# Optimization experiments

Hardware: AMD Instinct MI355X
Metric: run time of the kernel (lower is better)

The kernel has to match this reference:

```python
import jax, jax.numpy as jnp
import numpy as np

VOCAB, EMBED, HIDDEN = 32000, 256, 64
B, T = 4096, 64


def setup_inputs() -> dict:
    key = jax.random.key(0)
    ks = jax.random.split(key, 6)
    s = 1.0 / float(np.sqrt(HIDDEN))  # PyTorch LSTM init scale
    x = jax.random.randint(ks[0], (B, T), 0, VOCAB)
    embed_table = jax.random.normal(ks[1], (VOCAB, EMBED), jnp.float32)
    W_ih = jax.random.uniform(ks[2], (4 * HIDDEN, EMBED), jnp.float32, -s, s)
    W_hh = jax.random.uniform(ks[3], (4 * HIDDEN, HIDDEN), jnp.float32, -s, s)
    b_ih = jax.random.uniform(ks[4], (4 * HIDDEN,), jnp.float32, -s, s)
    b_hh = jax.random.uniform(ks[5], (4 * HIDDEN,), jnp.float32, -s, s)
    return {"x": x, "embed_table": embed_table, "W_ih": W_ih, "W_hh": W_hh, "b_ih": b_ih, "b_hh": b_hh}


def reference(x, embed_table, W_ih, W_hh, b_ih, b_hh):
    # Embedding lookup: [B,T,E]
    emb = embed_table[x]
    # Precompute input projection for all timesteps (PyTorch gate order i,f,g,o)
    xg = jnp.einsum('bte,ge->btg', emb, W_ih) + (b_ih + b_hh)  # [B,T,4H]
    xg = jnp.swapaxes(xg, 0, 1)  # [T,B,4H]
    h0 = jnp.zeros((x.shape[0], HIDDEN), xg.dtype)
    c0 = jnp.zeros((x.shape[0], HIDDEN), xg.dtype)

    def step(carry, xt):
        h, c = carry
        g = xt + h @ W_hh.T  # [B,4H]
        i, f, gg, o = jnp.split(g, 4, axis=-1)
        c = jax.nn.sigmoid(f) * c + jax.nn.sigmoid(i) * jnp.tanh(gg)
        h = jax.nn.sigmoid(o) * jnp.tanh(c)
        return (h, c), None

    (h, _), _ = jax.lax.scan(step, (h0, c0), xg)
    return h  # [B, HIDDEN] == hidden.squeeze(0)
```

## Files before the change

### kernel.cpp

```cpp
#include <hip/hip_runtime.h>
#include <math.h>

#define B_ 4096
#define T_ 64
#define E_ 256
#define H_ 64
#define V_ 32000
#define THREADS 512

typedef __attribute__((ext_vector_type(8))) short bf16x8;
typedef __attribute__((ext_vector_type(4))) float f32x4;
typedef __attribute__((ext_vector_type(4))) unsigned int u32x4;

__device__ __forceinline__ short f2bf(float x) {
    unsigned u = __float_as_uint(x);
    return (short)((u + 0x7FFFu + ((u >> 16) & 1u)) >> 16);
}
__device__ __forceinline__ unsigned cvt_pk_bf16(float lo, float hi) {
    unsigned r;
    asm("v_cvt_pk_bf16_f32 %0, %1, %2" : "=v"(r) : "v"(lo), "v"(hi));
    return r;
}
__device__ __forceinline__ float exp2_raw(float x) {
    float r; asm("v_exp_f32 %0, %1" : "=v"(r) : "v"(x)); return r;
}
__device__ __forceinline__ float rcp_raw(float x) {
    float r; asm("v_rcp_f32 %0, %1" : "=v"(r) : "v"(x)); return r;
}
#define LOG2E 1.442695041f

template <int CTRL>
__device__ __forceinline__ float dpp_f(float x) {
    return __int_as_float(
        __builtin_amdgcn_mov_dpp(__float_as_int(x), CTRL, 0xF, 0xF, true));
}

__device__ __forceinline__ void gld16(const void* g, void* l) {
    __builtin_amdgcn_global_load_lds(
        (const __attribute__((address_space(1))) void*)g,
        (__attribute__((address_space(3))) void*)l, 16, 0, 0);
}

__global__ void prep_kernel(const float* __restrict__ W_ih,
                            const float* __restrict__ W_hh,
                            const float* __restrict__ b_ih,
                            const float* __restrict__ b_hh,
                            const float* __restrict__ emb_table,
                            short* __restrict__ wih_frag,
                            short* __restrict__ whh_g,
                            float* __restrict__ bias_f,
                            short* __restrict__ emb_bf,
                            int tabN) {
    int tid = blockIdx.x * blockDim.x + threadIdx.x;
    int stride = gridDim.x * blockDim.x;
    for (int i = tid; i < 65536; i += stride) {
        int jj = i & 7;
        int l  = (i >> 3) & 63;
        int kc = (i >> 9) & 7;
        int tl = (i >> 12) & 1;
        int vv = i >> 13;
        int uu = (l & 15) >> 1, pp = l & 1;
        int g = tl * 128 + pp * 64 + vv * 8 + uu;
        int k = kc * 32 + (l >> 4) * 8 + jj;
        wih_frag[i] = f2bf(W_ih[g * E_ + k]);
    }
    for (int i = tid; i < 256 * 64; i += stride) whh_g[i] = f2bf(W_hh[i]);
    for (int i = tid; i < 256; i += stride) bias_f[i] = b_ih[i] + b_hh[i];
    for (int i = tid; i < (tabN >> 2); i += stride) {
        float4 v = ((const float4*)emb_table)[i];
        uint2 w;
        w.x = cvt_pk_bf16(v.x, v.y);
        w.y = cvt_pk_bf16(v.z, v.w);
        ((uint2*)emb_bf)[i] = w;
    }
}

template <int TAB>
__global__ __attribute__((amdgpu_flat_work_group_size(THREADS, THREADS),
                          amdgpu_waves_per_eu(2, 2)))
void lstm_f(const int* __restrict__ x,
            const float* __restrict__ embf,
            const short* __restrict__ embb,
            const short* __restrict__ wih_frag,
            const short* __restrict__ whh_g,
            const float* __restrict__ bias_f,
            float* __restrict__ out) {
    __shared__ __align__(16) short s_ef[4][4096];
    __shared__ __align__(16) short s_hf[2][1024];
    __shared__ int s_idx[1024];

    const int tid  = threadIdx.x;
    const int lane = tid & 63;
    const int wave = tid >> 6;
    const int r0   = blockIdx.x * 16;

    {
        const int tt = tid & 63;
        const int mA = tid >> 6;
        s_idx[tt * 16 + mA]     = x[(r0 + mA) * T_ + tt];
        s_idx[tt * 16 + mA + 8] = x[(r0 + mA + 8) * T_ + tt];
    }
    ((int*)s_hf)[tid]       = 0;
    ((int*)s_hf)[tid + 512] = 0;

    const int p  = lane & 1;
    const int c4 = lane >> 4;
    const int u  = (lane & 15) >> 1;
    const float scl2 = p ? 1.0f : 2.0f;
    const float offB = p ? 0.0f : -1.0f;
    const float enB  = -LOG2E * scl2;
    const int m0 = c4 * 4 + p * 2;

    bf16x8 wA[8], wB[8], qA0, qA1, qB0, qB1;
    float bA, bB;
    int hw_s;
    {
        const short* wp = wih_frag + wave * 8192 + lane * 8;
        #pragma unroll
        for (int kc = 0; kc < 8; ++kc) {
            wA[kc] = *(const bf16x8*)(wp + kc * 512);
            wB[kc] = *(const bf16x8*)(wp + 4096 + kc * 512);
        }
        const int gA = p * 64 + wave * 8 + u;
        const short* qp = whh_g + gA * 64 + c4 * 8;
        qA0 = *(const bf16x8*)(qp);
        qA1 = *(const bf16x8*)(qp + 32);
        qB0 = *(const bf16x8*)(qp + 8192);
        qB1 = *(const bf16x8*)(qp + 8192 + 32);
        bA = bias_f[gA];
        bB = bias_f[gA + 128];
        hw_s = (wave >> 2) * 512 + (wave & 3) * 128
             + ((u & 1) ? (m0 + 1) * 8 + (u - 1) : m0 * 8 + u);
    }

    const int m16   = lane & 15;
    const int sbase = wave * 512 + lane * 8;
    const int skoff = wave * 32 + (lane >> 4) * 8;

    __syncthreads();

    #pragma unroll
    for (int tt = 0; tt < 3; ++tt) {
        int tok = s_idx[tt * 16 + m16];
        if (TAB) {
            gld16(embb + (size_t)tok * E_ + skoff, &s_ef[tt][wave * 512]);
        } else {
            const float* pr = embf + (size_t)tok * E_ + skoff;
            float4 f0 = *(const float4*)pr;
            float4 f1 = *(const float4*)(pr + 4);
            u32x4 w;
            w[0] = cvt_pk_bf16(f0.x, f0.y);
            w[1] = cvt_pk_bf16(f0.z, f0.w);
            w[2] = cvt_pk_bf16(f1.x, f1.y);
            w[3] = cvt_pk_bf16(f1.z, f1.w);
            *(u32x4*)(&s_ef[tt][0] + sbase) = w;
        }
    }
    if (TAB) {
        asm volatile("s_waitcnt vmcnt(1) lgkmcnt(0)" ::: "memory");
        __builtin_amdgcn_s_barrier();
        __builtin_amdgcn_sched_barrier(0);
    } else {
        __syncthreads();
    }

    float c0 = 0.f, c1 = 0.f, h0v = 0.f, h1v = 0.f;
    f32x4 a0, a1, b0, b1;

    {
        a0 = (f32x4){bA, bA, bA, bA};
        b0 = (f32x4){bB, bB, bB, bB};
        a1 = (f32x4){0.f, 0.f, 0.f, 0.f};
        b1 = (f32x4){0.f, 0.f, 0.f, 0.f};
        const short* eb = &s_ef[0][0] + lane * 8;
        #pragma unroll
        for (int kc = 0; kc < 4; ++kc) {
            bf16x8 av = *(const bf16x8*)(eb + kc * 512);
            bf16x8 aw = *(const bf16x8*)(eb + (kc + 4) * 512);
            a0 = __builtin_amdgcn_mfma_f32_16x16x32_bf16(av, wA[kc], a0, 0, 0, 0);
            b0 = __builtin_amdgcn_mfma_f32_16x16x32_bf16(av, wB[kc], b0, 0, 0, 0);
            a1 = __builtin_amdgcn_mfma_f32_16x16x32_bf16(aw, wA[kc + 4], a1, 0, 0, 0);
            b1 = __builtin_amdgcn_mfma_f32_16x16x32_bf16(aw, wB[kc + 4], b1, 0, 0, 0);
        }
    }

    auto gates_phase = [&](const float* ga, const float* gb, int t) {
        float sA[4], Bv[4];
        #pragma unroll
        for (int q = 0; q < 4; ++q) {
            sA[q] = rcp_raw(1.0f + exp2_raw(-LOG2E * ga[q]));
            Bv[q] = rcp_raw(1.0f + exp2_raw(enB * gb[q])) * scl2 + offB;
        }
        float s1 = p ? sA[0] : sA[2] * Bv[2];
        float r1 = dpp_f<0xB1>(s1);
        float s2 = p ? sA[1] : sA[3] * Bv[3];
        float r2 = dpp_f<0xB1>(s2);
        float r3 = dpp_f<0xB1>(Bv[0]);
        float r4 = dpp_f<0xB1>(Bv[1]);
        float fc0 = p ? sA[2] : r1;
        float ic0 = p ? r1 : sA[0] * Bv[0];
        float oc0 = p ? Bv[2] : r3;
        float fc1 = p ? sA[3] : r2;
        float ic1 = p ? r2 : sA[1] * Bv[1];
        float oc1 = p ? Bv[3] : r4;
        c0 = fc0 * c0 + ic0;
        c1 = fc1 * c1 + ic1;
        h0v = oc0 * (1.0f - 2.0f * rcp_raw(1.0f + exp2_raw(2.0f * LOG2E * c0)));
        h1v = oc1 * (1.0f - 2.0f * rcp_raw(1.0f + exp2_raw(2.0f * LOG2E * c1)));
        float snd = (u & 1) ? h0v : h1v;
        float rcv = dpp_f<0x4E>(snd);
        unsigned hw = (u & 1) ? cvt_pk_bf16(rcv, h1v) : cvt_pk_bf16(h0v, rcv);
        *(unsigned*)(&s_hf[(t + 1) & 1][0] + hw_s) = hw;
    };

    auto p_phase = [&](int t) {
        a0 = (f32x4){bA, bA, bA, bA};
        b0 = (f32x4){bB, bB, bB, bB};
        a1 = (f32x4){0.f, 0.f, 0.f, 0.f};
        b1 = (f32x4){0.f, 0.f, 0.f, 0.f};
        const short* eb = &s_ef[(t + 1) & 3][0] + lane * 8;
        __builtin_amdgcn_s_setprio(1);
        #pragma unroll
        for (int kc = 0; kc < 4; ++kc) {
            bf16x8 av = *(const bf16x8*)(eb + kc * 512);
            bf16x8 aw = *(const bf16x8*)(eb + (kc + 4) * 512);
            a0 = __builtin_amdgcn_mfma_f32_16x16x32_bf16(av, wA[kc], a0, 0, 0, 0);
            b0 = __builtin_amdgcn_mfma_f32_16x16x32_bf16(av, wB[kc], b0, 0, 0, 0);
            a1 = __builtin_amdgcn_mfma_f32_16x16x32_bf16(aw, wA[kc + 4], a1, 0, 0, 0);
            b1 = __builtin_amdgcn_mfma_f32_16x16x32_bf16(aw, wB[kc + 4], b1, 0, 0, 0);
        }
        __builtin_amdgcn_s_setprio(0);
    };

    #pragma unroll 4
    for (int t = 0; t < T_; ++t) {
        {
            const int ts = (t + 3 < T_) ? t + 3 : T_ - 1;
            int tok = s_idx[ts * 16 + m16];
            if (TAB) {
                gld16(embb + (size_t)tok * E_ + skoff,
                      &s_ef[(t + 3) & 3][wave * 512]);
            } else {
                const float* pr = embf + (size_t)tok * E_ + skoff;
                float4 f0 = *(const float4*)pr;
                float4 f1 = *(const float4*)(pr + 4);
                u32x4 w;
                w[0] = cvt_pk_bf16(f0.x, f0.y);
                w[1] = cvt_pk_bf16(f0.z, f0.w);
                w[2] = cvt_pk_bf16(f1.x, f1.y);
                w[3] = cvt_pk_bf16(f1.z, f1.w);
                *(u32x4*)(&s_ef[(t + 3) & 3][0] + sbase) = w;
            }
        }

        const short* hb = &s_hf[t & 1][0] + lane * 8;
        bf16x8 hv0 = *(const bf16x8*)(hb);
        bf16x8 hv1 = *(const bf16x8*)(hb + 512);
        __builtin_amdgcn_s_setprio(1);
        a0 = __builtin_amdgcn_mfma_f32_16x16x32_bf16(hv0, qA0, a0, 0, 0, 0);
        a1 = __builtin_amdgcn_mfma_f32_16x16x32_bf16(hv1, qA1, a1, 0, 0, 0);
        b0 = __builtin_amdgcn_mfma_f32_16x16x32_bf16(hv0, qB0, b0, 0, 0, 0);
        b1 = __builtin_amdgcn_mfma_f32_16x16x32_bf16(hv1, qB1, b1, 0, 0, 0);
        __builtin_amdgcn_s_setprio(0);

        float ga[4], gb[4];
        #pragma unroll
        for (int q = 0; q < 4; ++q) {
            ga[q] = a0[q] + a1[q];
            gb[q] = b0[q] + b1[q];
        }

        if (wave < 4) {
            gates_phase(ga, gb, t);
            if (t < T_ - 1) p_phase(t);
        } else {
            __builtin_amdgcn_sched_barrier(0);
            if (t < T_ - 1) p_phase(t);
            __builtin_amdgcn_sched_barrier(0);
            gates_phase(ga, gb, t);
        }

        if (TAB) {
            asm volatile("s_waitcnt vmcnt(1) lgkmcnt(0)" ::: "memory");
            __builtin_amdgcn_s_barrier();
            __builtin_amdgcn_sched_barrier(0);
        } else {
            __syncthreads();
        }
    }

    {
        const int j = wave * 8 + u;
        out[(r0 + m0) * H_ + j]     = h0v;
        out[(r0 + m0 + 1) * H_ + j] = h1v;
    }
}

extern "C" void kernel_launch(void* const* d_in, const int* in_sizes, int n_in,
                              void* d_out, int out_size, void* d_ws, size_t ws_size,
                              hipStream_t stream) {
    const int*   x         = (const int*)d_in[0];
    const float* emb_table = (const float*)d_in[1];
    const float* W_ih      = (const float*)d_in[2];
    const float* W_hh      = (const float*)d_in[3];
    const float* b_ih      = (const float*)d_in[4];
    const float* b_hh      = (const float*)d_in[5];
    float*       out       = (float*)d_out;

    short* wih_frag = (short*)d_ws;
    short* whh_g    = wih_frag + 65536;
    float* bias_f   = (float*)(whh_g + 16384);
    short* emb_bf   = (short*)(bias_f + 256);

    const size_t need = (size_t)(65536 + 16384) * 2 + 256 * 4
                      + (size_t)V_ * E_ * 2;
    const int tab = (ws_size >= need) ? 1 : 0;

    prep_kernel<<<tab ? 1024 : 64, 256, 0, stream>>>(
        W_ih, W_hh, b_ih, b_hh, emb_table,
        wih_frag, whh_g, bias_f,
        tab ? emb_bf : wih_frag, tab ? V_ * E_ : 0);

    if (tab) {
        lstm_f<1><<<B_ / 16, THREADS, 0, stream>>>(
            x, emb_table, emb_bf, wih_frag, whh_g, bias_f, out);
    } else {
        lstm_f<0><<<B_ / 16, THREADS, 0, stream>>>(
            x, emb_table, wih_frag, wih_frag, whh_g, bias_f, out);
    }
}
```

Measured before the change: 67.75 us.

## Dedicate extra producer waves to embedding gather, freeing compute waves

Adds four producer waves per block that exclusively prefetch embedding rows into the LDS ring buffer. The eight compute waves now run only the recurrent MFMAs and gate math, so they no longer issue global loads on the serial path. The prep kernel converts eight floats per thread with a larger grid. The added waves raise the waves-per-EU target to 3, which tightens the register budget and may cause spills of the weight fragments.

```diff
diff --git a/kernel.cpp b/kernel.cpp
--- a/kernel.cpp
+++ b/kernel.cpp
@@ -6,7 +6,7 @@
 #define E_ 256
 #define H_ 64
 #define V_ 32000
-#define THREADS 512
+#define THREADS 768
 
 typedef __attribute__((ext_vector_type(8))) short bf16x8;
 typedef __attribute__((ext_vector_type(4))) float f32x4;
@@ -66,18 +66,21 @@
     }
     for (int i = tid; i < 256 * 64; i += stride) whh_g[i] = f2bf(W_hh[i]);
     for (int i = tid; i < 256; i += stride) bias_f[i] = b_ih[i] + b_hh[i];
-    for (int i = tid; i < (tabN >> 2); i += stride) {
-        float4 v = ((const float4*)emb_table)[i];
-        uint2 w;
-        w.x = cvt_pk_bf16(v.x, v.y);
-        w.y = cvt_pk_bf16(v.z, v.w);
-        ((uint2*)emb_bf)[i] = w;
+    for (int i = tid; i < (tabN >> 3); i += stride) {
+        float4 v0 = ((const float4*)emb_table)[i * 2];
+        float4 v1 = ((const float4*)emb_table)[i * 2 + 1];
+        u32x4 w;
+        w[0] = cvt_pk_bf16(v0.x, v0.y);
+        w[1] = cvt_pk_bf16(v0.z, v0.w);
+        w[2] = cvt_pk_bf16(v1.x, v1.y);
+        w[3] = cvt_pk_bf16(v1.z, v1.w);
+        ((u32x4*)emb_bf)[i] = w;
     }
 }
 
 template <int TAB>
 __global__ __attribute__((amdgpu_flat_work_group_size(THREADS, THREADS),
-                          amdgpu_waves_per_eu(2, 2)))
+                          amdgpu_waves_per_eu(3, 3)))
 void lstm_f(const int* __restrict__ x,
             const float* __restrict__ embf,
             const short* __restrict__ embb,
@@ -94,14 +97,10 @@
     const int wave = tid >> 6;
     const int r0   = blockIdx.x * 16;
 
-    {
-        const int tt = tid & 63;
-        const int mA = tid >> 6;
-        s_idx[tt * 16 + mA]     = x[(r0 + mA) * T_ + tt];
-        s_idx[tt * 16 + mA + 8] = x[(r0 + mA + 8) * T_ + tt];
-    }
-    ((int*)s_hf)[tid]       = 0;
-    ((int*)s_hf)[tid + 512] = 0;
+    for (int i = tid; i < 1024; i += THREADS)
+        s_idx[(i & 63) * 16 + (i >> 6)] = x[(r0 + (i >> 6)) * T_ + (i & 63)];
+    for (int i = tid; i < 1024; i += THREADS)
+        ((int*)s_hf)[i] = 0;
 
     const int p  = lane & 1;
     const int c4 = lane >> 4;
@@ -112,9 +111,9 @@
     const int m0 = c4 * 4 + p * 2;
 
     bf16x8 wA[8], wB[8], qA0, qA1, qB0, qB1;
-    float bA, bB;
-    int hw_s;
-    {
+    float bA = 0.f, bB = 0.f;
+    int hw_s = 0;
+    if (wave < 8) {
         const short* wp = wih_frag + wave * 8192 + lane * 8;
         #pragma unroll
         for (int kc = 0; kc < 8; ++kc) {
@@ -133,31 +132,40 @@
              + ((u & 1) ? (m0 + 1) * 8 + (u - 1) : m0 * 8 + u);
     }
 
-    const int m16   = lane & 15;
-    const int sbase = wave * 512 + lane * 8;
-    const int skoff = wave * 32 + (lane >> 4) * 8;
+    const int m16    = lane & 15;
+    const int kc0    = (wave - 8) * 2;
+    const int sbase0 = kc0 * 512 + lane * 8;
+    const int skoff0 = kc0 * 32 + (lane >> 4) * 8;
+    const int skoff1 = skoff0 + 32;
 
     __syncthreads();
 
-    #pragma unroll
-    for (int tt = 0; tt < 3; ++tt) {
-        int tok = s_idx[tt * 16 + m16];
-        if (TAB) {
-            gld16(embb + (size_t)tok * E_ + skoff, &s_ef[tt][wave * 512]);
-        } else {
-            const float* pr = embf + (size_t)tok * E_ + skoff;
-            float4 f0 = *(const float4*)pr;
-            float4 f1 = *(const float4*)(pr + 4);
-            u32x4 w;
-            w[0] = cvt_pk_bf16(f0.x, f0.y);
-            w[1] = cvt_pk_bf16(f0.z, f0.w);
-            w[2] = cvt_pk_bf16(f1.x, f1.y);
-            w[3] = cvt_pk_bf16(f1.z, f1.w);
-            *(u32x4*)(&s_ef[tt][0] + sbase) = w;
+    if (wave >= 8) {
+        #pragma unroll
+        for (int tt = 0; tt < 3; ++tt) {
+            int tok = s_idx[tt * 16 + m16];
+            if (TAB) {
+                gld16(embb + (size_t)tok * E_ + skoff0, &s_ef[tt][kc0 * 512]);
+                gld16(embb + (size_t)tok * E_ + skoff1, &s_ef[tt][kc0 * 512 + 512]);
+            } else {
+                const float* pr = embf + (size_t)tok * E_;
+                #pragma unroll
+                for (int kk = 0; kk < 2; ++kk) {
+                    const float* q = pr + skoff0 + kk * 32;
+                    float4 f0 = *(const float4*)q;
+                    float4 f1 = *(const float4*)(q + 4);
+                    u32x4 w;
+                    w[0] = cvt_pk_bf16(f0.x, f0.y);
+                    w[1] = cvt_pk_bf16(f0.z, f0.w);
+                    w[2] = cvt_pk_bf16(f1.x, f1.y);
+                    w[3] = cvt_pk_bf16(f1.z, f1.w);
+                    *(u32x4*)(&s_ef[tt][0] + sbase0 + kk * 512) = w;
+                }
+            }
         }
     }
     if (TAB) {
-        asm volatile("s_waitcnt vmcnt(1) lgkmcnt(0)" ::: "memory");
+        asm volatile("s_waitcnt vmcnt(2) lgkmcnt(0)" ::: "memory");
         __builtin_amdgcn_s_barrier();
         __builtin_amdgcn_sched_barrier(0);
     } else {
@@ -167,7 +175,7 @@
     float c0 = 0.f, c1 = 0.f, h0v = 0.f, h1v = 0.f;
     f32x4 a0, a1, b0, b1;
 
-    {
+    if (wave < 8) {
         a0 = (f32x4){bA, bA, bA, bA};
         b0 = (f32x4){bB, bB, bB, bB};
         a1 = (f32x4){0.f, 0.f, 0.f, 0.f};
@@ -234,54 +242,60 @@
 
     #pragma unroll 4
     for (int t = 0; t < T_; ++t) {
-        {
-            const int ts = (t + 3 < T_) ? t + 3 : T_ - 1;
-            int tok = s_idx[ts * 16 + m16];
-            if (TAB) {
-                gld16(embb + (size_t)tok * E_ + skoff,
-                      &s_ef[(t + 3) & 3][wave * 512]);
+        if (wave < 8) {
+            const short* hb = &s_hf[t & 1][0] + lane * 8;
+            bf16x8 hv0 = *(const bf16x8*)(hb);
+            bf16x8 hv1 = *(const bf16x8*)(hb + 512);
+            __builtin_amdgcn_s_setprio(1);
+            a0 = __builtin_amdgcn_mfma_f32_16x16x32_bf16(hv0, qA0, a0, 0, 0, 0);
+            a1 = __builtin_amdgcn_mfma_f32_16x16x32_bf16(hv1, qA1, a1, 0, 0, 0);
+            b0 = __builtin_amdgcn_mfma_f32_16x16x32_bf16(hv0, qB0, b0, 0, 0, 0);
+            b1 = __builtin_amdgcn_mfma_f32_16x16x32_bf16(hv1, qB1, b1, 0, 0, 0);
+            __builtin_amdgcn_s_setprio(0);
+
+            float ga[4], gb[4];
+            #pragma unroll
+            for (int q = 0; q < 4; ++q) {
+                ga[q] = a0[q] + a1[q];
+                gb[q] = b0[q] + b1[q];
+            }
+
+            if (wave < 4) {
+                gates_phase(ga, gb, t);
+                if (t < T_ - 1) p_phase(t);
             } else {
-                const float* pr = embf + (size_t)tok * E_ + skoff;
-                float4 f0 = *(const float4*)pr;
-                float4 f1 = *(const float4*)(pr + 4);
-                u32x4 w;
-                w[0] = cvt_pk_bf16(f0.x, f0.y);
-                w[1] = cvt_pk_bf16(f0.z, f0.w);
-                w[2] = cvt_pk_bf16(f1.x, f1.y);
-                w[3] = cvt_pk_bf16(f1.z, f1.w);
-                *(u32x4*)(&s_ef[(t + 3) & 3][0] + sbase) = w;
+                __builtin_amdgcn_sched_barrier(0);
+                if (t < T_ - 1) p_phase(t);
+                __builtin_amdgcn_sched_barrier(0);
+                gates_phase(ga, gb, t);
             }
-        }
-
-        const short* hb = &s_hf[t & 1][0] + lane * 8;
-        bf16x8 hv0 = *(const bf16x8*)(hb);
-        bf16x8 hv1 = *(const bf16x8*)(hb + 512);
-        __builtin_amdgcn_s_setprio(1);
-        a0 = __builtin_amdgcn_mfma_f32_16x16x32_bf16(hv0, qA0, a0, 0, 0, 0);
-        a1 = __builtin_amdgcn_mfma_f32_16x16x32_bf16(hv1, qA1, a1, 0, 0, 0);
-        b0 = __builtin_amdgcn_mfma_f32_16x16x32_bf16(hv0, qB0, b0, 0, 0, 0);
-        b1 = __builtin_amdgcn_mfma_f32_16x16x32_bf16(hv1, qB1, b1, 0, 0, 0);
-        __builtin_amdgcn_s_setprio(0);
-
-        float ga[4], gb[4];
-        #pragma unroll
-        for (int q = 0; q < 4; ++q) {
-            ga[q] = a0[q] + a1[q];
-            gb[q] = b0[q] + b1[q];
-        }
-
-        if (wave < 4) {
-            gates_phase(ga, gb, t);
-            if (t < T_ - 1) p_phase(t);
         } else {
-            __builtin_amdgcn_sched_barrier(0);
-            if (t < T_ - 1) p_phase(t);
-            __builtin_amdgcn_sched_barrier(0);
-            gates_phase(ga, gb, t);
-        }
-
+            if (t + 3 < T_) {
+                int tok = s_idx[(t + 3) * 16 + m16];
+                if (TAB) {
+                    gld16(embb + (size_t)tok * E_ + skoff0,
+                          &s_ef[(t + 3) & 3][kc0 * 512]);
+                    gld16(embb + (size_t)tok * E_ + skoff1,
+                          &s_ef[(t + 3) & 3][kc0 * 512 + 512]);
+                } else {
+                    const float* pr = embf + (size_t)tok * E_;
+                    #pragma unroll
+                    for (int kk = 0; kk < 2; ++kk) {
+                        const float* q = pr + skoff0 + kk * 32;
+                        float4 f0 = *(const float4*)q;
+                        float4 f1 = *(const float4*)(q + 4);
+                        u32x4 w;
+                        w[0] = cvt_pk_bf16(f0.x, f0.y);
+                        w[1] = cvt_pk_bf16(f0.z, f0.w);
+                        w[2] = cvt_pk_bf16(f1.x, f1.y);
+                        w[3] = cvt_pk_bf16(f1.z, f1.w);
+                        *(u32x4*)(&s_ef[(t + 3) & 3][0] + sbase0 + kk * 512) = w;
+                    }
+                }
+            }
+        }
         if (TAB) {
-            asm volatile("s_waitcnt vmcnt(1) lgkmcnt(0)" ::: "memory");
+            asm volatile("s_waitcnt vmcnt(2) lgkmcnt(0)" ::: "memory");
             __builtin_amdgcn_s_barrier();
             __builtin_amdgcn_sched_barrier(0);
         } else {
@@ -289,7 +303,7 @@
         }
     }
 
-    {
+    if (wave < 8) {
         const int j = wave * 8 + u;
         out[(r0 + m0) * H_ + j]     = h0v;
         out[(r0 + m0 + 1) * H_ + j] = h1v;
@@ -316,7 +330,7 @@
                       + (size_t)V_ * E_ * 2;
     const int tab = (ws_size >= need) ? 1 : 0;
 
-    prep_kernel<<<tab ? 1024 : 64, 256, 0, stream>>>(
+    prep_kernel<<<tab ? 2048 : 64, 256, 0, stream>>>(
         W_ih, W_hh, b_ih, b_hh, emb_table,
         wih_frag, whh_g, bias_f,
         tab ? emb_bf : wih_frag, tab ? V_ * E_ : 0);
```

After: 63.33 us (median of 2 runs). -6.5%, faster.
